# Optimization experiments

Hardware: AMD Instinct MI355X
Metric: run time of the kernel (lower is better)

Reference implementation:

```python
import jax, jax.numpy as jnp
import numpy as np

N_NODES = 50000
N_EDGES = 800000
D = 128


def _sage_conv(x, src, dst, W_l, b_l, W_r):
    # PyG SAGEConv (mean aggr): out = lin_l(mean_{j in N(i)} x_j) + lin_r(x_i)
    # lin_l has bias, lin_r does not.
    msg = x[src]                                             # [E, D] gather
    agg = jax.ops.segment_sum(msg, dst, num_segments=N_NODES)  # [N, D] scatter-add
    cnt = jax.ops.segment_sum(jnp.ones((src.shape[0],), x.dtype), dst,
                              num_segments=N_NODES)          # [N]
    mean = agg / jnp.maximum(cnt, 1.0)[:, None]
    return mean @ W_l.T + b_l + x @ W_r.T


def setup_inputs() -> dict:
    key = jax.random.key(0)
    ks = jax.random.split(key, 12)
    x = jax.random.normal(ks[0], (N_NODES, D), dtype=jnp.float32)
    edge_index = jax.random.randint(ks[1], (2, N_EDGES), 0, N_NODES, dtype=jnp.int64)
    s = 1.0 / np.sqrt(D)
    params = {}
    for i, layer in enumerate((1, 2, 3)):
        params[f"W_l{layer}"] = jax.random.uniform(ks[2 + 3 * i], (D, D), jnp.float32, -s, s)
        params[f"b_l{layer}"] = jax.random.uniform(ks[3 + 3 * i], (D,), jnp.float32, -s, s)
        params[f"W_r{layer}"] = jax.random.uniform(ks[4 + 3 * i], (D, D), jnp.float32, -s, s)
    return {"x": x, "edge_index": edge_index, **params}


def reference(x, edge_index, W_l1, b_l1, W_r1, W_l2, b_l2, W_r2, W_l3, b_l3, W_r3):
    src, dst = edge_index[0], edge_index[1]
    h = jax.nn.relu(_sage_conv(x, src, dst, W_l1, b_l1, W_r1))
    # F.dropout(x) in the source defaults to training=True; treated as
    # identity (eval mode) for a deterministic correctness baseline.
    h = _sage_conv(h, src, dst, W_l2, b_l2, W_r2)
    h = _sage_conv(h, src, dst, W_l3, b_l3, W_r3)
    return h
```

## Files before the change

kernel.cpp:

```cpp
#include <hip/hip_runtime.h>
#include <hip/hip_fp16.h>

constexpr int D = 128;
constexpr int SLOT = 64;

typedef _Float16 half_t;
typedef __attribute__((ext_vector_type(8))) _Float16 half8;
typedef __attribute__((ext_vector_type(4))) _Float16 half4;
typedef __attribute__((ext_vector_type(4))) float f32x4;


__device__ __forceinline__ void wpk_item(const float* __restrict__ Wl,
                                         const float* __restrict__ Wr,
                                         half_t* __restrict__ Wpk, int idx) {
    int j = idx & 7;
    int lanei = (idx >> 3) & 63;
    int frag = idx >> 9;
    int kc = frag >> 3, nf = frag & 7;
    int k = kc * 32 + (lanei >> 4) * 8 + j;
    int c = nf * 16 + (lanei & 15);
    float v = (k < D) ? Wl[c * D + k] : Wr[c * D + (k - D)];
    Wpk[idx] = (half_t)v;
}


__global__ void preamble_kernel(const int* __restrict__ src, const int* __restrict__ dst,
                                int* __restrict__ cnt, int* __restrict__ ssrc, int E,
                                const float* __restrict__ x, half_t* __restrict__ x_h, int n4,
                                const float* __restrict__ Wl1, const float* __restrict__ Wr1, half_t* __restrict__ Wpk1,
                                const float* __restrict__ Wl2, const float* __restrict__ Wr2, half_t* __restrict__ Wpk2,
                                const float* __restrict__ Wl3, const float* __restrict__ Wr3, half_t* __restrict__ Wpk3,
                                int FB8, int VB, int WB) {
    int b = blockIdx.x;
    int tid = threadIdx.x;
    if (b < FB8) {
        int p = b & 7;
        int e = (b >> 3) * 256 + tid;
        if (e < E) {
            int d = dst[e];
            if ((d & 7) == p) {
                int rank = atomicAdd(&cnt[d], 1);
                if (rank < SLOT) ssrc[d * SLOT + rank] = src[e];
            }
        }
        return;
    }
    b -= FB8;
    if (b < VB) {
        int i = b * 256 + tid;
        if (i < n4) {
            float4 v = ((const float4*)x)[i];
            half4 h;
            h[0] = (half_t)v.x; h[1] = (half_t)v.y; h[2] = (half_t)v.z; h[3] = (half_t)v.w;
            ((half4*)x_h)[i] = h;
        }
        return;
    }
    b -= VB;
    int which = b / WB;
    int idx = (b % WB) * 256 + tid;
    if (idx < 2 * D * D) {
        if (which == 0)      wpk_item(Wl1, Wr1, Wpk1, idx);
        else if (which == 1) wpk_item(Wl2, Wr2, Wpk2, idx);
        else                 wpk_item(Wl3, Wr3, Wpk3, idx);
    }
}


__global__ void agg_kernel(const half_t* __restrict__ hin, const int* __restrict__ cnt,
                           const int* __restrict__ ssrc, half_t* __restrict__ mean, int n) {
    int node = blockIdx.x * (blockDim.x >> 6) + (threadIdx.x >> 6);
    if (node >= n) return;
    int lane = threadIdx.x & 63;
    int g = lane >> 4;
    int c = lane & 15;
    int cn = cnt[node];
    int deg = (cn < SLOT) ? cn : SLOT;
    const int* row = ssrc + (size_t)node * SLOT;
    const half8* hp = (const half8*)hin;

    half8 a0, a1, a2, a3;
    #pragma unroll
    for (int k = 0; k < 8; ++k) { a0[k] = (half_t)0.f; a1[k] = (half_t)0.f;
                                  a2[k] = (half_t)0.f; a3[k] = (half_t)0.f; }

    int j = g;
    for (; j + 12 < deg; j += 16) {
        int s0 = row[j];
        int s1 = row[j + 4];
        int s2 = row[j + 8];
        int s3 = row[j + 12];
        a0 += hp[(size_t)s0 * 16 + c];
        a1 += hp[(size_t)s1 * 16 + c];
        a2 += hp[(size_t)s2 * 16 + c];
        a3 += hp[(size_t)s3 * 16 + c];
    }
    for (; j < deg; j += 4) {
        int s0 = row[j];
        a0 += hp[(size_t)s0 * 16 + c];
    }
    half8 m = (a0 + a1) + (a2 + a3);

    #pragma unroll
    for (int off = 16; off <= 32; off <<= 1) {
        half8 t;
        int* mp = (int*)&m;
        int* tp = (int*)&t;
        #pragma unroll
        for (int k = 0; k < 4; ++k) tp[k] = __shfl_xor(mp[k], off, 64);
        m += t;
    }

    if (g == 0) {
        float inv = 1.0f / (float)(cn > 1 ? cn : 1);
        half8 o;
        #pragma unroll
        for (int k = 0; k < 8; ++k) o[k] = (half_t)((float)m[k] * inv);
        ((half8*)mean)[(size_t)node * 16 + c] = o;
    }
}


template <int RELU, int FINAL>
__global__ __launch_bounds__(256) void gemm_kernel(
    const half_t* __restrict__ meanh, const half_t* __restrict__ hin,
    const half_t* __restrict__ Wpk, const float* __restrict__ bias,
    float* __restrict__ out_f32, half_t* __restrict__ out_f16, int nrows) {
    int wave = threadIdx.x >> 6;
    int lane = threadIdx.x & 63;
    int m0 = blockIdx.x * 128 + wave * 32;
    int r = lane & 15;
    int kb = lane >> 4;
    int row0 = m0 + r;
    int row1 = m0 + 16 + r;
    int rc0 = (row0 < nrows) ? row0 : 0;
    int rc1 = (row1 < nrows) ? row1 : 0;

    f32x4 acc[2][8];
    #pragma unroll
    for (int i = 0; i < 2; ++i)
        #pragma unroll
        for (int nf = 0; nf < 8; ++nf) acc[i][nf] = f32x4{0.f, 0.f, 0.f, 0.f};

    const half8* wp = (const half8*)Wpk;
    #pragma unroll
    for (int kc = 0; kc < 8; ++kc) {
        const half_t* s0 = (kc < 4)
            ? (meanh + (size_t)rc0 * D + kc * 32 + kb * 8)
            : (hin   + (size_t)rc0 * D + (kc - 4) * 32 + kb * 8);
        const half_t* s1 = (kc < 4)
            ? (meanh + (size_t)rc1 * D + kc * 32 + kb * 8)
            : (hin   + (size_t)rc1 * D + (kc - 4) * 32 + kb * 8);
        half8 a0 = *(const half8*)s0;
        half8 a1 = *(const half8*)s1;
        #pragma unroll
        for (int nf = 0; nf < 8; ++nf) {
            half8 b = wp[(kc * 8 + nf) * 64 + lane];
            acc[0][nf] = __builtin_amdgcn_mfma_f32_16x16x32_f16(a0, b, acc[0][nf], 0, 0, 0);
            acc[1][nf] = __builtin_amdgcn_mfma_f32_16x16x32_f16(a1, b, acc[1][nf], 0, 0, 0);
        }
    }

    int colb = lane & 15;
    int rbase = (lane >> 4) * 4;
    #pragma unroll
    for (int nf = 0; nf < 8; ++nf) {
        int col = nf * 16 + colb;
        float bv = bias[col];
        #pragma unroll
        for (int i = 0; i < 2; ++i) {
            #pragma unroll
            for (int rr = 0; rr < 4; ++rr) {
                int orow = m0 + i * 16 + rbase + rr;
                if (orow < nrows) {
                    float v = acc[i][nf][rr] + bv;
                    if (RELU) v = fmaxf(v, 0.f);
                    if (FINAL) out_f32[(size_t)orow * D + col] = v;
                    else       out_f16[(size_t)orow * D + col] = (half_t)v;
                }
            }
        }
    }
}


extern "C" void kernel_launch(void* const* d_in, const int* in_sizes, int n_in,
                              void* d_out, int out_size, void* d_ws, size_t ws_size,
                              hipStream_t stream) {
    const float* x   = (const float*)d_in[0];
    const int*   ei  = (const int*)d_in[1];
    const float* Wl1 = (const float*)d_in[2];
    const float* bl1 = (const float*)d_in[3];
    const float* Wr1 = (const float*)d_in[4];
    const float* Wl2 = (const float*)d_in[5];
    const float* bl2 = (const float*)d_in[6];
    const float* Wr2 = (const float*)d_in[7];
    const float* Wl3 = (const float*)d_in[8];
    const float* bl3 = (const float*)d_in[9];
    const float* Wr3 = (const float*)d_in[10];
    float* out = (float*)d_out;

    const int N = in_sizes[0] / D;
    const int E = in_sizes[1] / 2;

    char* ws = (char*)d_ws;
    size_t off = 0;
    auto alloc = [&](size_t bytes) -> void* {
        off = (off + 255) & ~(size_t)255;
        void* p = ws + off;
        off += bytes;
        return p;
    };
    half_t* x_h   = (half_t*)alloc((size_t)N * D * 2);
    half_t* meanh = (half_t*)alloc((size_t)N * D * 2);
    half_t* h_a   = (half_t*)alloc((size_t)N * D * 2);
    half_t* h_b   = (half_t*)alloc((size_t)N * D * 2);
    half_t* Wpk1  = (half_t*)alloc((size_t)2 * D * D * 2);
    half_t* Wpk2  = (half_t*)alloc((size_t)2 * D * D * 2);
    half_t* Wpk3  = (half_t*)alloc((size_t)2 * D * D * 2);
    int*   cnt  = (int*)alloc((size_t)N * 4);
    int*   ssrc = (int*)alloc((size_t)N * SLOT * 4);

    const int* srcp = ei;
    const int* dstp = ei + E;

    const int FB8 = 8 * ((E + 255) / 256);
    const int n4 = N * D / 4;
    const int VB = (n4 + 255) / 256;
    const int WB = (2 * D * D + 255) / 256;

    hipMemsetAsync(cnt, 0, (size_t)N * 4, stream);
    preamble_kernel<<<FB8 + VB + 3 * WB, 256, 0, stream>>>(
        srcp, dstp, cnt, ssrc, E, x, x_h, n4,
        Wl1, Wr1, Wpk1, Wl2, Wr2, Wpk2, Wl3, Wr3, Wpk3, FB8, VB, WB);

    int aggBlocks  = (N + 3) / 4;
    int gemmBlocks = (N + 127) / 128;

    agg_kernel<<<aggBlocks, 256, 0, stream>>>(x_h, cnt, ssrc, meanh, N);
    gemm_kernel<1, 0><<<gemmBlocks, 256, 0, stream>>>(meanh, x_h, Wpk1, bl1, nullptr, h_a, N);

    agg_kernel<<<aggBlocks, 256, 0, stream>>>(h_a, cnt, ssrc, meanh, N);
    gemm_kernel<0, 0><<<gemmBlocks, 256, 0, stream>>>(meanh, h_a, Wpk2, bl2, nullptr, h_b, N);

    agg_kernel<<<aggBlocks, 256, 0, stream>>>(h_b, cnt, ssrc, meanh, N);
    gemm_kernel<0, 1><<<gemmBlocks, 256, 0, stream>>>(meanh, h_b, Wpk3, bl3, out, nullptr, N);
}
```

Before: 278.4 us.

## Fuse neighbor mean aggregation into the per-layer MFMA GEMM kernel via LDS

Merges the separate aggregation and GEMM kernels into a single per-layer kernel. Each block computes mean-aggregated rows for 64 nodes into swizzled shared memory, then runs the MFMA GEMM reading the mean half from LDS. This removes the global round trip of the mean buffer and three kernel launches. In exchange, aggregation switches from 4 subgroups per node to one 16-lane group per node with int4 index loads, which lowers the memory-level parallelism per node. Each wave also now handles 16 rows instead of 32, so fewer MFMAs reuse each weight load.

```diff
diff --git a/kernel.cpp b/kernel.cpp
--- a/kernel.cpp
+++ b/kernel.cpp
@@ -67,117 +67,95 @@
 }
 
 
-__global__ void agg_kernel(const half_t* __restrict__ hin, const int* __restrict__ cnt,
-                           const int* __restrict__ ssrc, half_t* __restrict__ mean, int n) {
-    int node = blockIdx.x * (blockDim.x >> 6) + (threadIdx.x >> 6);
-    if (node >= n) return;
-    int lane = threadIdx.x & 63;
-    int g = lane >> 4;
-    int c = lane & 15;
-    int cn = cnt[node];
-    int deg = (cn < SLOT) ? cn : SLOT;
-    const int* row = ssrc + (size_t)node * SLOT;
-    const half8* hp = (const half8*)hin;
-
-    half8 a0, a1, a2, a3;
-    #pragma unroll
-    for (int k = 0; k < 8; ++k) { a0[k] = (half_t)0.f; a1[k] = (half_t)0.f;
-                                  a2[k] = (half_t)0.f; a3[k] = (half_t)0.f; }
-
-    int j = g;
-    for (; j + 12 < deg; j += 16) {
-        int s0 = row[j];
-        int s1 = row[j + 4];
-        int s2 = row[j + 8];
-        int s3 = row[j + 12];
-        a0 += hp[(size_t)s0 * 16 + c];
-        a1 += hp[(size_t)s1 * 16 + c];
-        a2 += hp[(size_t)s2 * 16 + c];
-        a3 += hp[(size_t)s3 * 16 + c];
-    }
-    for (; j < deg; j += 4) {
-        int s0 = row[j];
-        a0 += hp[(size_t)s0 * 16 + c];
-    }
-    half8 m = (a0 + a1) + (a2 + a3);
-
-    #pragma unroll
-    for (int off = 16; off <= 32; off <<= 1) {
-        half8 t;
-        int* mp = (int*)&m;
-        int* tp = (int*)&t;
-        #pragma unroll
-        for (int k = 0; k < 4; ++k) tp[k] = __shfl_xor(mp[k], off, 64);
-        m += t;
-    }
-
-    if (g == 0) {
-        float inv = 1.0f / (float)(cn > 1 ? cn : 1);
-        half8 o;
-        #pragma unroll
-        for (int k = 0; k < 8; ++k) o[k] = (half_t)((float)m[k] * inv);
-        ((half8*)mean)[(size_t)node * 16 + c] = o;
-    }
-}
-
-
 template <int RELU, int FINAL>
-__global__ __launch_bounds__(256) void gemm_kernel(
-    const half_t* __restrict__ meanh, const half_t* __restrict__ hin,
-    const half_t* __restrict__ Wpk, const float* __restrict__ bias,
+__global__ __launch_bounds__(256) void layer_kernel(
+    const half_t* __restrict__ hin, const int* __restrict__ cnt,
+    const int* __restrict__ ssrc, const half_t* __restrict__ Wpk,
+    const float* __restrict__ bias,
     float* __restrict__ out_f32, half_t* __restrict__ out_f16, int nrows) {
-    int wave = threadIdx.x >> 6;
-    int lane = threadIdx.x & 63;
-    int m0 = blockIdx.x * 128 + wave * 32;
+    __shared__ half_t mlds[64 * D];
+    int tid = threadIdx.x;
+    int lane = tid & 63;
+    int wave = tid >> 6;
+    int block0 = blockIdx.x * 64;
+
+    {
+        int sg = tid >> 4;
+        int c  = tid & 15;
+        const half8* hp = (const half8*)hin;
+        for (int rr = 0; rr < 4; ++rr) {
+            int r = sg * 4 + rr;
+            int node = block0 + r;
+            half8 o;
+            #pragma unroll
+            for (int k = 0; k < 8; ++k) o[k] = (half_t)0.f;
+            if (node < nrows) {
+                int cn = cnt[node];
+                int deg = (cn < SLOT) ? cn : SLOT;
+                const int* row = ssrc + (size_t)node * SLOT;
+                half8 a0 = o, a1 = o, a2 = o, a3 = o;
+                int j = 0;
+                for (; j + 3 < deg; j += 4) {
+                    int4 ss = *(const int4*)&row[j];
+                    a0 += hp[(size_t)ss.x * 16 + c];
+                    a1 += hp[(size_t)ss.y * 16 + c];
+                    a2 += hp[(size_t)ss.z * 16 + c];
+                    a3 += hp[(size_t)ss.w * 16 + c];
+                }
+                for (; j < deg; ++j) a0 += hp[(size_t)row[j] * 16 + c];
+                half8 m = (a0 + a1) + (a2 + a3);
+                float inv = 1.0f / (float)(cn > 1 ? cn : 1);
+                #pragma unroll
+                for (int k = 0; k < 8; ++k) o[k] = (half_t)((float)m[k] * inv);
+            }
+            int byte = (r * 256 + c * 16) ^ ((r & 7) << 4);
+            *(half8*)((char*)mlds + byte) = o;
+        }
+    }
+    __syncthreads();
+
     int r = lane & 15;
     int kb = lane >> 4;
-    int row0 = m0 + r;
-    int row1 = m0 + 16 + r;
-    int rc0 = (row0 < nrows) ? row0 : 0;
-    int rc1 = (row1 < nrows) ? row1 : 0;
-
-    f32x4 acc[2][8];
+    int trow = wave * 16 + r;
+    int grow = block0 + trow;
+    int rowc = (grow < nrows) ? grow : 0;
+
+    f32x4 acc[8];
     #pragma unroll
-    for (int i = 0; i < 2; ++i)
-        #pragma unroll
-        for (int nf = 0; nf < 8; ++nf) acc[i][nf] = f32x4{0.f, 0.f, 0.f, 0.f};
+    for (int nf = 0; nf < 8; ++nf) acc[nf] = f32x4{0.f, 0.f, 0.f, 0.f};
 
     const half8* wp = (const half8*)Wpk;
     #pragma unroll
     for (int kc = 0; kc < 8; ++kc) {
-        const half_t* s0 = (kc < 4)
-            ? (meanh + (size_t)rc0 * D + kc * 32 + kb * 8)
-            : (hin   + (size_t)rc0 * D + (kc - 4) * 32 + kb * 8);
-        const half_t* s1 = (kc < 4)
-            ? (meanh + (size_t)rc1 * D + kc * 32 + kb * 8)
-            : (hin   + (size_t)rc1 * D + (kc - 4) * 32 + kb * 8);
-        half8 a0 = *(const half8*)s0;
-        half8 a1 = *(const half8*)s1;
+        half8 a;
+        if (kc < 4) {
+            int byte = (trow * 256 + kc * 64 + kb * 16) ^ ((trow & 7) << 4);
+            a = *(const half8*)((char*)mlds + byte);
+        } else {
+            a = *(const half8*)(hin + (size_t)rowc * D + (kc - 4) * 32 + kb * 8);
+        }
         #pragma unroll
         for (int nf = 0; nf < 8; ++nf) {
             half8 b = wp[(kc * 8 + nf) * 64 + lane];
-            acc[0][nf] = __builtin_amdgcn_mfma_f32_16x16x32_f16(a0, b, acc[0][nf], 0, 0, 0);
-            acc[1][nf] = __builtin_amdgcn_mfma_f32_16x16x32_f16(a1, b, acc[1][nf], 0, 0, 0);
+            acc[nf] = __builtin_amdgcn_mfma_f32_16x16x32_f16(a, b, acc[nf], 0, 0, 0);
         }
     }
 
     int colb = lane & 15;
     int rbase = (lane >> 4) * 4;
+    int m0 = block0 + wave * 16;
     #pragma unroll
     for (int nf = 0; nf < 8; ++nf) {
         int col = nf * 16 + colb;
         float bv = bias[col];
         #pragma unroll
-        for (int i = 0; i < 2; ++i) {
-            #pragma unroll
-            for (int rr = 0; rr < 4; ++rr) {
-                int orow = m0 + i * 16 + rbase + rr;
-                if (orow < nrows) {
-                    float v = acc[i][nf][rr] + bv;
-                    if (RELU) v = fmaxf(v, 0.f);
-                    if (FINAL) out_f32[(size_t)orow * D + col] = v;
-                    else       out_f16[(size_t)orow * D + col] = (half_t)v;
-                }
+        for (int rr = 0; rr < 4; ++rr) {
+            int orow = m0 + rbase + rr;
+            if (orow < nrows) {
+                float v = acc[nf][rr] + bv;
+                if (RELU) v = fmaxf(v, 0.f);
+                if (FINAL) out_f32[(size_t)orow * D + col] = v;
+                else       out_f16[(size_t)orow * D + col] = (half_t)v;
             }
         }
     }
@@ -212,7 +190,6 @@
         return p;
     };
     half_t* x_h   = (half_t*)alloc((size_t)N * D * 2);
-    half_t* meanh = (half_t*)alloc((size_t)N * D * 2);
     half_t* h_a   = (half_t*)alloc((size_t)N * D * 2);
     half_t* h_b   = (half_t*)alloc((size_t)N * D * 2);
     half_t* Wpk1  = (half_t*)alloc((size_t)2 * D * D * 2);
@@ -234,15 +211,9 @@
         srcp, dstp, cnt, ssrc, E, x, x_h, n4,
         Wl1, Wr1, Wpk1, Wl2, Wr2, Wpk2, Wl3, Wr3, Wpk3, FB8, VB, WB);
 
-    int aggBlocks  = (N + 3) / 4;
-    int gemmBlocks = (N + 127) / 128;
-
-    agg_kernel<<<aggBlocks, 256, 0, stream>>>(x_h, cnt, ssrc, meanh, N);
-    gemm_kernel<1, 0><<<gemmBlocks, 256, 0, stream>>>(meanh, x_h, Wpk1, bl1, nullptr, h_a, N);
-
-    agg_kernel<<<aggBlocks, 256, 0, stream>>>(h_a, cnt, ssrc, meanh, N);
-    gemm_kernel<0, 0><<<gemmBlocks, 256, 0, stream>>>(meanh, h_a, Wpk2, bl2, nullptr, h_b, N);
-
-    agg_kernel<<<aggBlocks, 256, 0, stream>>>(h_b, cnt, ssrc, meanh, N);
-    gemm_kernel<0, 1><<<gemmBlocks, 256, 0, stream>>>(meanh, h_b, Wpk3, bl3, out, nullptr, N);
-}
+    int layerBlocks = (N + 63) / 64;
+
+    layer_kernel<1, 0><<<layerBlocks, 256, 0, stream>>>(x_h, cnt, ssrc, Wpk1, bl1, nullptr, h_a, N);
+    layer_kernel<0, 0><<<layerBlocks, 256, 0, stream>>>(h_a, cnt, ssrc, Wpk2, bl2, nullptr, h_b, N);
+    layer_kernel<0, 1><<<layerBlocks, 256, 0, stream>>>(h_b, cnt, ssrc, Wpk3, bl3, out, nullptr, N);
+}
```

After: 265.5 us. -4.6%, faster.
